# Kernel tuning notes

Measured on AMD Instinct MI355X. Metric: run time of the kernel, lower is better.

The kernel has to match this reference:

```python
import jax, jax.numpy as jnp
import numpy as np

B, L, H, R = 8, 128, 768, 24


def setup_inputs() -> dict:
    key = jax.random.key(0)
    ks = jax.random.split(key, 12)
    s = 0.02  # init scale
    f32 = jnp.float32
    inp = {
        "embed_tokens": jax.random.normal(ks[0], (B, L, H), f32),
        "attention_mask": jnp.ones((B, L), f32),
        "target_rel": jax.random.randint(ks[1], (B,), 0, R),
        # relation-judgement head
        "W_hr": jax.random.normal(ks[2], (H, H // 2), f32) * s,
        "b_hr": jnp.zeros((H // 2,), f32),
        "W_rj": jax.random.normal(ks[3], (H // 2, R), f32) * s,
        "b_rj": jnp.zeros((R,), f32),
        # relation embedding
        "rel_emb": jax.random.normal(ks[4], (R, H), f32) * s,
        # correspondence matrix head (input is concat -> 2H)
        "W_corr": jax.random.normal(ks[5], (2 * H, H), f32) * s,
        "b_corr": jnp.zeros((H,), f32),
        "W_gc": jax.random.normal(ks[6], (H, 1), f32) * s,
        "b_gc": jnp.zeros((1,), f32),
        # subject tagging head (fusion_type='concat' -> 2H in, H hidden)
        "W_sh": jax.random.normal(ks[7], (2 * H, H), f32) * s,
        "b_sh": jnp.zeros((H,), f32),
        "W_st": jax.random.normal(ks[8], (H, 3), f32) * s,
        "b_st": jnp.zeros((3,), f32),
        # object tagging head
        "W_oh": jax.random.normal(ks[9], (2 * H, H), f32) * s,
        "b_oh": jnp.zeros((H,), f32),
        "W_ot": jax.random.normal(ks[10], (H, 3), f32) * s,
        "b_ot": jnp.zeros((3,), f32),
    }
    return inp


def reference(embed_tokens, attention_mask, target_rel,
              W_hr, b_hr, W_rj, b_rj, rel_emb,
              W_corr, b_corr, W_gc, b_gc,
              W_sh, b_sh, W_st, b_st,
              W_oh, b_oh, W_ot, b_ot):
    # ---- stage 1: masked mean-pool + relation judgement (dropout = identity at inference)
    masked = embed_tokens * attention_mask[:, :, None]            # [B,L,H]
    pool = jnp.sum(masked, axis=1) / jnp.sum(attention_mask, axis=1)[:, None]  # [B,H]
    rel_hidden = jax.nn.relu(pool @ W_hr + b_hr)                  # [B,H/2]
    stage1 = rel_hidden @ W_rj + b_rj                             # [B,R]

    # ---- correspondence matrix: concat[b,i,j] = [embed[b,j], embed[b,i]]
    # Decompose concat-linear: concat @ W_corr = embed_j @ W1 + embed_i @ W2
    W1, W2 = W_corr[:H_dim(embed_tokens)], W_corr[H_dim(embed_tokens):]
    A = embed_tokens @ W1                                         # [B,L,H] (j-index part)
    C = embed_tokens @ W2                                         # [B,L,H] (i-index part)
    corres_hidden = jax.nn.relu(A[:, None, :, :] + C[:, :, None, :] + b_corr)  # [B,L,L,H]
    pred_corres = corres_hidden @ W_gc + b_gc                     # [B,L,L,1]

    # ---- relation-fused tagging (mode == 'train')
    re = rel_emb[target_rel]                                      # [B,H]
    Bsz, Lsz, Hsz = embed_tokens.shape
    fusion = jnp.concatenate(
        [jnp.broadcast_to(re[:, None, :], (Bsz, Lsz, Hsz)), embed_tokens], axis=-1)  # [B,L,2H]
    subj = jax.nn.relu(fusion @ W_sh + b_sh) @ W_st + b_st        # [B,L,3]
    obj = jax.nn.relu(fusion @ W_oh + b_oh) @ W_ot + b_ot         # [B,L,3]

    return stage1, subj, obj, pred_corres


def H_dim(x):
    return x.shape[-1]
```

## Files before the change

kernel.cpp:

```cpp
#include <hip/hip_runtime.h>
#include <hip/hip_bf16.h>

#define BD   8
#define LD   128
#define HD   768
#define RD   24
#define H2D  384
#define NF   1536
#define WSZ  589824

typedef __attribute__((ext_vector_type(8))) short bf16x8;
typedef __attribute__((ext_vector_type(4))) float f32x4;

__device__ __forceinline__ short f2bf(float f) {
    __hip_bfloat16 h = __float2bfloat16(f);
    return *reinterpret_cast<short*>(&h);
}

__global__ __launch_bounds__(256) void prep_kernel(
        const float* __restrict__ embed, const float* __restrict__ mask,
        const float* __restrict__ rel_emb, const int* __restrict__ trel,
        const float* __restrict__ W_corr,
        const float* __restrict__ W_sh, const float* __restrict__ b_sh,
        const float* __restrict__ W_oh, const float* __restrict__ b_oh,
        const float* __restrict__ b_st, const float* __restrict__ b_ot,
        float* __restrict__ pool, float* __restrict__ biasrel,
        unsigned short* __restrict__ embedB, unsigned short* __restrict__ WT,
        float* __restrict__ out_subj, float* __restrict__ out_obj) {
    const int q = blockIdx.x, tid = threadIdx.x;

    if (q < 96) {
        const int b = q / 12, c = q % 12;
        __shared__ float mrow[LD];
        __shared__ float msum;
        __shared__ float part[4][64];
        if (tid < LD) mrow[tid] = mask[b * LD + tid];
        __syncthreads();
        if (tid == 0) {
            float s = 0.f;
            for (int l = 0; l < LD; ++l) s += mrow[l];
            msum = s;
        }
        __syncthreads();
        const int lc = tid >> 6, hh = tid & 63;
        const int h = c * 64 + hh;
        float acc = 0.f;
        const float* base = embed + ((size_t)b * LD + lc * 32) * HD + h;
#pragma unroll 8
        for (int i = 0; i < 32; ++i) acc += base[(size_t)i * HD] * mrow[lc * 32 + i];
        part[lc][hh] = acc;
        __syncthreads();
        if (lc == 0)
            pool[b * HD + h] = (part[0][hh] + part[1][hh] + part[2][hh] + part[3][hh]) / msum;
    } else if (q < 192) {
        const int qq = q - 96;
        const int b = qq / 12, cc = qq % 12;
        __shared__ float re[HD];
        __shared__ float part2[2][128];
        const int rel = trel[b];
        for (int k = tid; k < HD; k += 256) re[k] = rel_emb[(size_t)rel * HD + k];
        if (qq == 0 && tid < 3 * LD) {
            const int l = tid / 3, t = tid - 3 * l;
            out_subj[(l) * 3 + t] = b_st[t];
            out_obj [(l) * 3 + t] = b_ot[t];
        }
        if (cc == 0 && b > 0 && tid < 3 * LD) {
            const int l = tid / 3, t = tid - 3 * l;
            out_subj[(b * LD + l) * 3 + t] = b_st[t];
            out_obj [(b * LD + l) * 3 + t] = b_ot[t];
        }
        __syncthreads();
        const int kc = tid >> 7, nn = tid & 127;
        const int n = cc * 128 + nn;
        const float* Wp; float bb; int col;
        if (n < HD) { Wp = W_sh; bb = b_sh[n];      col = n; }
        else        { Wp = W_oh; bb = b_oh[n - HD]; col = n - HD; }
        float acc = 0.f;
#pragma unroll 8
        for (int i = 0; i < 384; ++i) {
            const int k = kc * 384 + i;
            acc += re[k] * Wp[(size_t)k * HD + col];
        }
        part2[kc][nn] = acc;
        __syncthreads();
        if (kc == 0) biasrel[b * NF + n] = part2[0][nn] + part2[1][nn] + bb;
    } else if (q < 288) {
        const int base = (q - 192) * 8192;
#pragma unroll
        for (int it = 0; it < 4; ++it) {
            const int off = base + it * 2048 + tid * 8;
            float4 v0 = *(const float4*)&embed[off];
            float4 v1 = *(const float4*)&embed[off + 4];
            bf16x8 p;
            p[0] = f2bf(v0.x); p[1] = f2bf(v0.y); p[2] = f2bf(v0.z); p[3] = f2bf(v0.w);
            p[4] = f2bf(v1.x); p[5] = f2bf(v1.y); p[6] = f2bf(v1.z); p[7] = f2bf(v1.w);
            *(bf16x8*)&embedB[off] = p;
        }
    } else {
        const int qq = q - 288;
        const int w = qq / 144, t = qq % 144;
        const int kt = t / 12, nt = t % 12;
        const float* src = (w == 0) ? W_corr
                         : (w == 1) ? W_corr + WSZ
                         : (w == 2) ? W_sh + WSZ
                                    : W_oh + WSZ;
        unsigned short* dst = WT + (size_t)w * WSZ;
        __shared__ float tile[64 * 65];
        const int r = tid >> 2, c4 = (tid & 3) * 16;
#pragma unroll
        for (int i = 0; i < 4; ++i) {
            float4 v = *(const float4*)&src[(size_t)(kt * 64 + r) * HD + nt * 64 + c4 + i * 4];
            tile[r * 65 + c4 + i * 4 + 0] = v.x;
            tile[r * 65 + c4 + i * 4 + 1] = v.y;
            tile[r * 65 + c4 + i * 4 + 2] = v.z;
            tile[r * 65 + c4 + i * 4 + 3] = v.w;
        }
        __syncthreads();
        bf16x8 p0, p1;
#pragma unroll
        for (int j = 0; j < 8; ++j) {
            p0[j] = f2bf(tile[(c4 + j) * 65 + r]);
            p1[j] = f2bf(tile[(c4 + 8 + j) * 65 + r]);
        }
        unsigned short* o = dst + (size_t)(nt * 64 + r) * HD + kt * 64 + c4;
        *(bf16x8*)(o)     = p0;
        *(bf16x8*)(o + 8) = p1;
    }
}

__global__ __launch_bounds__(256) void biggemm(
        const unsigned short* __restrict__ embedB,
        const unsigned short* __restrict__ WT,
        const float* __restrict__ biasrel,
        const float* __restrict__ W_st, const float* __restrict__ W_ot,
        const float* __restrict__ pool,
        const float* __restrict__ W_hr, const float* __restrict__ b_hr,
        float* __restrict__ AC, float* __restrict__ out_subj,
        float* __restrict__ out_obj, float* __restrict__ rh) {
    const int tid = threadIdx.x;

    if (blockIdx.x >= 24) {
        const int b = blockIdx.y >> 1;
        const int c = (blockIdx.x - 24) * 2 + (blockIdx.y & 1);
        __shared__ float prow[HD];
        __shared__ float rpart[4][64];
        for (int k = tid; k < HD; k += 256) prow[k] = pool[b * HD + k];
        __syncthreads();
        const int kc = tid >> 6, nn = tid & 63;
        const int n = c * 64 + nn;
        float acc = 0.f;
#pragma unroll 8
        for (int i = 0; i < 192; ++i) {
            const int k = kc * 192 + i;
            acc += prow[k] * W_hr[(size_t)k * H2D + n];
        }
        rpart[kc][nn] = acc;
        __syncthreads();
        if (kc == 0)
            rh[b * H2D + n] = fmaxf(rpart[0][nn] + rpart[1][nn] + rpart[2][nn] + rpart[3][nn] + b_hr[n], 0.f);
        return;
    }

    __shared__ __align__(16) short As [64][40];
    __shared__ __align__(16) short Bs0[64][40];
    __shared__ __align__(16) short Bs1[64][40];
    __shared__ float partial[64][3];

    const int bn0 = blockIdx.x * 64;
    const int bm0 = blockIdx.y * 64;

    const unsigned short* W0 = (bn0 < HD) ? WT : WT + WSZ;
    const unsigned short* W1 = (bn0 < HD) ? WT + 2 * (size_t)WSZ : WT + 3 * (size_t)WSZ;
    const int col0 = (bn0 < HD) ? bn0 : bn0 - HD;

    if (tid < 192) partial[tid / 3][tid % 3] = 0.f;

    const int row = tid >> 2;
    const int kc8 = (tid & 3) * 8;

    const int lane = tid & 63;
    const int wv = tid >> 6;
    const int wm = (wv >> 1) * 32;
    const int wn = (wv & 1) * 32;
    const int fr = lane & 15;
    const int kq = (lane >> 4) * 8;
    const int mq = (lane >> 4) * 4;

    f32x4 c00 = {0.f,0.f,0.f,0.f}, c01 = c00, c10 = c00, c11 = c00;
    f32x4 h00 = c00, h01 = c00, h10 = c00, h11 = c00;

    for (int kt = 0; kt < 24; ++kt) {
        const int k0 = kt << 5;
        bf16x8 av = *(const bf16x8*)&embedB[(size_t)(bm0 + row) * HD + k0 + kc8];
        bf16x8 b0v = *(const bf16x8*)&W0[(size_t)(col0 + row) * HD + k0 + kc8];
        bf16x8 b1v = *(const bf16x8*)&W1[(size_t)(col0 + row) * HD + k0 + kc8];

        __syncthreads();
        *(bf16x8*)&As [row][kc8] = av;
        *(bf16x8*)&Bs0[row][kc8] = b0v;
        *(bf16x8*)&Bs1[row][kc8] = b1v;
        __syncthreads();

        bf16x8 a0 = *(bf16x8*)&As[wm + fr][kq];
        bf16x8 a1 = *(bf16x8*)&As[wm + 16 + fr][kq];
        bf16x8 b0 = *(bf16x8*)&Bs0[wn + fr][kq];
        bf16x8 b1 = *(bf16x8*)&Bs0[wn + 16 + fr][kq];
        bf16x8 d0 = *(bf16x8*)&Bs1[wn + fr][kq];
        bf16x8 d1 = *(bf16x8*)&Bs1[wn + 16 + fr][kq];
        c00 = __builtin_amdgcn_mfma_f32_16x16x32_bf16(a0, b0, c00, 0, 0, 0);
        c01 = __builtin_amdgcn_mfma_f32_16x16x32_bf16(a0, b1, c01, 0, 0, 0);
        c10 = __builtin_amdgcn_mfma_f32_16x16x32_bf16(a1, b0, c10, 0, 0, 0);
        c11 = __builtin_amdgcn_mfma_f32_16x16x32_bf16(a1, b1, c11, 0, 0, 0);
        h00 = __builtin_amdgcn_mfma_f32_16x16x32_bf16(a0, d0, h00, 0, 0, 0);
        h01 = __builtin_amdgcn_mfma_f32_16x16x32_bf16(a0, d1, h01, 0, 0, 0);
        h10 = __builtin_amdgcn_mfma_f32_16x16x32_bf16(a1, d0, h10, 0, 0, 0);
        h11 = __builtin_amdgcn_mfma_f32_16x16x32_bf16(a1, d1, h11, 0, 0, 0);
    }

#pragma unroll
    for (int i = 0; i < 2; ++i) {
#pragma unroll
        for (int j = 0; j < 2; ++j) {
            f32x4 a = (i == 0) ? (j == 0 ? c00 : c01) : (j == 0 ? c10 : c11);
            const int ncol = bn0 + wn + j * 16 + fr;
#pragma unroll
            for (int r = 0; r < 4; ++r) {
                const int mrow = bm0 + wm + i * 16 + mq + r;
                AC[(size_t)mrow * NF + ncol] = a[r];
            }
        }
    }

    {
        const float* brl = biasrel + (size_t)(bm0 / LD) * NF;
        const float* Wt = (bn0 < HD) ? W_st : W_ot;
        float* op = (bn0 < HD) ? out_subj : out_obj;
        float pt[8][3] = {};
#pragma unroll
        for (int j = 0; j < 2; ++j) {
            const int ncol = bn0 + wn + j * 16 + fr;
            const int ncl = (bn0 < HD) ? ncol : ncol - HD;
            const float wt0 = Wt[ncl * 3 + 0];
            const float wt1 = Wt[ncl * 3 + 1];
            const float wt2 = Wt[ncl * 3 + 2];
            const float bias = brl[ncol];
#pragma unroll
            for (int i = 0; i < 2; ++i) {
                f32x4 a = (i == 0) ? (j == 0 ? h00 : h01) : (j == 0 ? h10 : h11);
#pragma unroll
                for (int r = 0; r < 4; ++r) {
                    const float v = fmaxf(a[r] + bias, 0.f);
                    pt[i * 4 + r][0] += v * wt0;
                    pt[i * 4 + r][1] += v * wt1;
                    pt[i * 4 + r][2] += v * wt2;
                }
            }
        }
#pragma unroll
        for (int mask = 1; mask < 16; mask <<= 1) {
#pragma unroll
            for (int x = 0; x < 8; ++x)
#pragma unroll
                for (int t = 0; t < 3; ++t)
                    pt[x][t] += __shfl_xor(pt[x][t], mask, 64);
        }
        if (fr == 0) {
#pragma unroll
            for (int i = 0; i < 2; ++i)
#pragma unroll
                for (int r = 0; r < 4; ++r)
#pragma unroll
                    for (int t = 0; t < 3; ++t)
                        atomicAdd(&partial[wm + i * 16 + mq + r][t], pt[i * 4 + r][t]);
        }
        __syncthreads();
        if (tid < 192) {
            const int m = tid / 3, t = tid % 3;
            atomicAdd(&op[(size_t)(bm0 + m) * 3 + t], partial[m][t]);
        }
    }
}

__global__ __launch_bounds__(512) void corres_kernel(
        const float* __restrict__ AC,
        const float* __restrict__ b_corr, const float* __restrict__ W_gc,
        const float* __restrict__ b_gc,
        const float* __restrict__ rh,
        const float* __restrict__ W_rj, const float* __restrict__ b_rj,
        float* __restrict__ out, float* __restrict__ out_stage1) {
    const int b = blockIdx.y;
    const int tid = threadIdx.x;

    if (blockIdx.x == 32) {
        __shared__ float rl[H2D];
        __shared__ float spart[8][RD];
        if (tid < H2D) rl[tid] = rh[b * H2D + tid];
        __syncthreads();
        if (tid < 8 * RD) {
            const int n = tid % RD, kc = tid / RD;
            float acc = 0.f;
#pragma unroll 8
            for (int i = 0; i < 48; ++i) {
                const int k = kc * 48 + i;
                acc += rl[k] * W_rj[k * RD + n];
            }
            spart[kc][n] = acc;
        }
        __syncthreads();
        if (tid < RD) {
            float s = b_rj[tid];
#pragma unroll
            for (int q = 0; q < 8; ++q) s += spart[q][tid];
            out_stage1[b * RD + tid] = s;
        }
        return;
    }

    const int i0 = blockIdx.x * 4;
    const int lane = tid & 63;
    const int wave = tid >> 6;

    f32x4 wg[3], cb[4][3];
#pragma unroll
    for (int s = 0; s < 3; ++s) {
        const int h = s * 256 + lane * 4;
        f32x4 w = *(const f32x4*)&W_gc[h];
        f32x4 bc = *(const f32x4*)&b_corr[h];
        wg[s] = w;
#pragma unroll
        for (int i = 0; i < 4; ++i) {
            f32x4 cv = *(const f32x4*)&AC[((size_t)(b * LD + i0 + i)) * NF + HD + h];
            cb[i][s] = cv + bc;
        }
    }
    const float bg = b_gc[0];

    for (int j = wave; j < LD; j += 8) {
        const float* arow = AC + ((size_t)(b * LD + j)) * NF;
        f32x4 a[3];
#pragma unroll
        for (int s = 0; s < 3; ++s) a[s] = *(const f32x4*)&arow[s * 256 + lane * 4];
        float sum[4] = {0.f, 0.f, 0.f, 0.f};
#pragma unroll
        for (int s = 0; s < 3; ++s) {
#pragma unroll
            for (int i = 0; i < 4; ++i) {
                f32x4 v = a[s] + cb[i][s];
#pragma unroll
                for (int t = 0; t < 4; ++t)
                    sum[i] += fmaxf(v[t], 0.f) * wg[s][t];
            }
        }
#pragma unroll
        for (int off = 32; off > 0; off >>= 1) {
#pragma unroll
            for (int i = 0; i < 4; ++i) sum[i] += __shfl_down(sum[i], off, 64);
        }
        if (lane == 0) {
#pragma unroll
            for (int i = 0; i < 4; ++i)
                out[((size_t)(b * LD + i0 + i)) * LD + j] = sum[i] + bg;
        }
    }
}

extern "C" void kernel_launch(void* const* d_in, const int* in_sizes, int n_in,
                              void* d_out, int out_size, void* d_ws, size_t ws_size,
                              hipStream_t stream) {
    const float* embed   = (const float*)d_in[0];
    const float* mask    = (const float*)d_in[1];
    const int*   trel    = (const int*)d_in[2];
    const float* W_hr    = (const float*)d_in[3];
    const float* b_hr    = (const float*)d_in[4];
    const float* W_rj    = (const float*)d_in[5];
    const float* b_rj    = (const float*)d_in[6];
    const float* rel_emb = (const float*)d_in[7];
    const float* W_corr  = (const float*)d_in[8];
    const float* b_corr  = (const float*)d_in[9];
    const float* W_gc    = (const float*)d_in[10];
    const float* b_gc    = (const float*)d_in[11];
    const float* W_sh    = (const float*)d_in[12];
    const float* b_sh    = (const float*)d_in[13];
    const float* W_st    = (const float*)d_in[14];
    const float* b_st    = (const float*)d_in[15];
    const float* W_oh    = (const float*)d_in[16];
    const float* b_oh    = (const float*)d_in[17];
    const float* W_ot    = (const float*)d_in[18];
    const float* b_ot    = (const float*)d_in[19];
    float* out = (float*)d_out;

    float* ws      = (float*)d_ws;
    float* AC      = ws;
    float* biasrel = ws + 1572864;
    float* rh      = ws + 1572864 + 12288;
    float* pool    = ws + 1572864 + 12288 + 3072;
    unsigned short* embedB = (unsigned short*)(ws + 1594368);
    unsigned short* WT     = (unsigned short*)(ws + 1594368 + 393216);

    float* out_stage1 = out;
    float* out_subj   = out + 192;
    float* out_obj    = out + 3264;
    float* out_corr   = out + 6336;

    prep_kernel<<<864, 256, 0, stream>>>(embed, mask, rel_emb, trel, W_corr,
                                         W_sh, b_sh, W_oh, b_oh, b_st, b_ot,
                                         pool, biasrel, embedB, WT,
                                         out_subj, out_obj);

    biggemm<<<dim3(27, 16), 256, 0, stream>>>(embedB, WT, biasrel, W_st, W_ot,
                                              pool, W_hr, b_hr,
                                              AC, out_subj, out_obj, rh);

    corres_kernel<<<dim3(33, BD), 512, 0, stream>>>(AC, b_corr, W_gc, b_gc,
                                                    rh, W_rj, b_rj, out_corr, out_stage1);
}
```

Measured before the change: 161.1 us.

## Fuse three kernels into one cooperative persistent kernel with grid syncs

Replaces the prep, GEMM and correspondence launches with a single cooperative kernel of 256 blocks that loops over the work units and uses grid-wide syncs between phases. If the cooperative launch fails, it falls back to three separate kernels. The correspondence stage also drops from 512 to 256 threads and prefetches the next AC row in registers. This removes launch gaps and tail effects, at the cost of fewer resident blocks per phase and the overhead of grid sync.

```diff
diff --git a/kernel.cpp b/kernel.cpp
--- a/kernel.cpp
+++ b/kernel.cpp
@@ -1,5 +1,8 @@
 #include <hip/hip_runtime.h>
 #include <hip/hip_bf16.h>
+#include <hip/hip_cooperative_groups.h>
+
+namespace cg = cooperative_groups;
 
 #define BD   8
 #define LD   128
@@ -17,110 +20,112 @@
     return *reinterpret_cast<short*>(&h);
 }
 
-__global__ __launch_bounds__(256) void prep_kernel(
-        const float* __restrict__ embed, const float* __restrict__ mask,
-        const float* __restrict__ rel_emb, const int* __restrict__ trel,
-        const float* __restrict__ W_corr,
-        const float* __restrict__ W_sh, const float* __restrict__ b_sh,
-        const float* __restrict__ W_oh, const float* __restrict__ b_oh,
-        const float* __restrict__ b_st, const float* __restrict__ b_ot,
-        float* __restrict__ pool, float* __restrict__ biasrel,
-        unsigned short* __restrict__ embedB, unsigned short* __restrict__ WT,
-        float* __restrict__ out_subj, float* __restrict__ out_obj) {
-    const int q = blockIdx.x, tid = threadIdx.x;
-
+struct KParams {
+    const float *embed, *mask;
+    const int *trel;
+    const float *W_hr, *b_hr, *W_rj, *b_rj, *rel_emb, *W_corr;
+    const float *b_corr, *W_gc, *b_gc;
+    const float *W_sh, *b_sh, *W_st, *b_st, *W_oh, *b_oh, *W_ot, *b_ot;
+    float *AC, *biasrel, *rh, *pool;
+    unsigned short *embedB, *WT;
+    float *out_stage1, *out_subj, *out_obj, *out_corr;
+};
+
+union SMem {
+    struct { float mrow[LD]; float msum; float part[4][64]; } pl;
+    struct { float re[HD]; float part2[2][128]; } br;
+    float tile[64 * 65];
+    struct __align__(16) { short As[64][40]; short Bs0[64][40]; short Bs1[64][40];
+                           float partial[64][3]; } gm;
+    struct { float prow[HD]; float rpart[4][64]; } rl;
+    struct { float rlb[H2D]; float spart[8][RD]; } st;
+};
+
+__device__ void prep_unit(const KParams& p, SMem& sm, int q, int tid) {
     if (q < 96) {
         const int b = q / 12, c = q % 12;
-        __shared__ float mrow[LD];
-        __shared__ float msum;
-        __shared__ float part[4][64];
-        if (tid < LD) mrow[tid] = mask[b * LD + tid];
+        if (tid < LD) sm.pl.mrow[tid] = p.mask[b * LD + tid];
         __syncthreads();
         if (tid == 0) {
             float s = 0.f;
-            for (int l = 0; l < LD; ++l) s += mrow[l];
-            msum = s;
+            for (int l = 0; l < LD; ++l) s += sm.pl.mrow[l];
+            sm.pl.msum = s;
         }
         __syncthreads();
         const int lc = tid >> 6, hh = tid & 63;
         const int h = c * 64 + hh;
         float acc = 0.f;
-        const float* base = embed + ((size_t)b * LD + lc * 32) * HD + h;
+        const float* base = p.embed + ((size_t)b * LD + lc * 32) * HD + h;
 #pragma unroll 8
-        for (int i = 0; i < 32; ++i) acc += base[(size_t)i * HD] * mrow[lc * 32 + i];
-        part[lc][hh] = acc;
+        for (int i = 0; i < 32; ++i) acc += base[(size_t)i * HD] * sm.pl.mrow[lc * 32 + i];
+        sm.pl.part[lc][hh] = acc;
         __syncthreads();
         if (lc == 0)
-            pool[b * HD + h] = (part[0][hh] + part[1][hh] + part[2][hh] + part[3][hh]) / msum;
+            p.pool[b * HD + h] = (sm.pl.part[0][hh] + sm.pl.part[1][hh] +
+                                  sm.pl.part[2][hh] + sm.pl.part[3][hh]) / sm.pl.msum;
     } else if (q < 192) {
         const int qq = q - 96;
         const int b = qq / 12, cc = qq % 12;
-        __shared__ float re[HD];
-        __shared__ float part2[2][128];
-        const int rel = trel[b];
-        for (int k = tid; k < HD; k += 256) re[k] = rel_emb[(size_t)rel * HD + k];
-        if (qq == 0 && tid < 3 * LD) {
-            const int l = tid / 3, t = tid - 3 * l;
-            out_subj[(l) * 3 + t] = b_st[t];
-            out_obj [(l) * 3 + t] = b_ot[t];
-        }
-        if (cc == 0 && b > 0 && tid < 3 * LD) {
-            const int l = tid / 3, t = tid - 3 * l;
-            out_subj[(b * LD + l) * 3 + t] = b_st[t];
-            out_obj [(b * LD + l) * 3 + t] = b_ot[t];
+        const int rel = p.trel[b];
+        for (int k = tid; k < HD; k += 256) sm.br.re[k] = p.rel_emb[(size_t)rel * HD + k];
+        if (cc == 0) {
+            for (int u = tid; u < 3 * LD; u += 256) {
+                const int l = u / 3, t = u - 3 * l;
+                p.out_subj[(b * LD + l) * 3 + t] = p.b_st[t];
+                p.out_obj [(b * LD + l) * 3 + t] = p.b_ot[t];
+            }
         }
         __syncthreads();
         const int kc = tid >> 7, nn = tid & 127;
         const int n = cc * 128 + nn;
         const float* Wp; float bb; int col;
-        if (n < HD) { Wp = W_sh; bb = b_sh[n];      col = n; }
-        else        { Wp = W_oh; bb = b_oh[n - HD]; col = n - HD; }
+        if (n < HD) { Wp = p.W_sh; bb = p.b_sh[n];      col = n; }
+        else        { Wp = p.W_oh; bb = p.b_oh[n - HD]; col = n - HD; }
         float acc = 0.f;
 #pragma unroll 8
         for (int i = 0; i < 384; ++i) {
             const int k = kc * 384 + i;
-            acc += re[k] * Wp[(size_t)k * HD + col];
-        }
-        part2[kc][nn] = acc;
-        __syncthreads();
-        if (kc == 0) biasrel[b * NF + n] = part2[0][nn] + part2[1][nn] + bb;
+            acc += sm.br.re[k] * Wp[(size_t)k * HD + col];
+        }
+        sm.br.part2[kc][nn] = acc;
+        __syncthreads();
+        if (kc == 0) p.biasrel[b * NF + n] = sm.br.part2[0][nn] + sm.br.part2[1][nn] + bb;
     } else if (q < 288) {
         const int base = (q - 192) * 8192;
 #pragma unroll
         for (int it = 0; it < 4; ++it) {
             const int off = base + it * 2048 + tid * 8;
-            float4 v0 = *(const float4*)&embed[off];
-            float4 v1 = *(const float4*)&embed[off + 4];
-            bf16x8 p;
-            p[0] = f2bf(v0.x); p[1] = f2bf(v0.y); p[2] = f2bf(v0.z); p[3] = f2bf(v0.w);
-            p[4] = f2bf(v1.x); p[5] = f2bf(v1.y); p[6] = f2bf(v1.z); p[7] = f2bf(v1.w);
-            *(bf16x8*)&embedB[off] = p;
+            float4 v0 = *(const float4*)&p.embed[off];
+            float4 v1 = *(const float4*)&p.embed[off + 4];
+            bf16x8 pk;
+            pk[0] = f2bf(v0.x); pk[1] = f2bf(v0.y); pk[2] = f2bf(v0.z); pk[3] = f2bf(v0.w);
+            pk[4] = f2bf(v1.x); pk[5] = f2bf(v1.y); pk[6] = f2bf(v1.z); pk[7] = f2bf(v1.w);
+            *(bf16x8*)&p.embedB[off] = pk;
         }
     } else {
         const int qq = q - 288;
         const int w = qq / 144, t = qq % 144;
         const int kt = t / 12, nt = t % 12;
-        const float* src = (w == 0) ? W_corr
-                         : (w == 1) ? W_corr + WSZ
-                         : (w == 2) ? W_sh + WSZ
-                                    : W_oh + WSZ;
-        unsigned short* dst = WT + (size_t)w * WSZ;
-        __shared__ float tile[64 * 65];
+        const float* src = (w == 0) ? p.W_corr
+                         : (w == 1) ? p.W_corr + WSZ
+                         : (w == 2) ? p.W_sh + WSZ
+                                    : p.W_oh + WSZ;
+        unsigned short* dst = p.WT + (size_t)w * WSZ;
         const int r = tid >> 2, c4 = (tid & 3) * 16;
 #pragma unroll
         for (int i = 0; i < 4; ++i) {
             float4 v = *(const float4*)&src[(size_t)(kt * 64 + r) * HD + nt * 64 + c4 + i * 4];
-            tile[r * 65 + c4 + i * 4 + 0] = v.x;
-            tile[r * 65 + c4 + i * 4 + 1] = v.y;
-            tile[r * 65 + c4 + i * 4 + 2] = v.z;
-            tile[r * 65 + c4 + i * 4 + 3] = v.w;
+            sm.tile[r * 65 + c4 + i * 4 + 0] = v.x;
+            sm.tile[r * 65 + c4 + i * 4 + 1] = v.y;
+            sm.tile[r * 65 + c4 + i * 4 + 2] = v.z;
+            sm.tile[r * 65 + c4 + i * 4 + 3] = v.w;
         }
         __syncthreads();
         bf16x8 p0, p1;
 #pragma unroll
         for (int j = 0; j < 8; ++j) {
-            p0[j] = f2bf(tile[(c4 + j) * 65 + r]);
-            p1[j] = f2bf(tile[(c4 + 8 + j) * 65 + r]);
+            p0[j] = f2bf(sm.tile[(c4 + j) * 65 + r]);
+            p1[j] = f2bf(sm.tile[(c4 + 8 + j) * 65 + r]);
         }
         unsigned short* o = dst + (size_t)(nt * 64 + r) * HD + kt * 64 + c4;
         *(bf16x8*)(o)     = p0;
@@ -128,56 +133,18 @@
     }
 }
 
-__global__ __launch_bounds__(256) void biggemm(
-        const unsigned short* __restrict__ embedB,
-        const unsigned short* __restrict__ WT,
-        const float* __restrict__ biasrel,
-        const float* __restrict__ W_st, const float* __restrict__ W_ot,
-        const float* __restrict__ pool,
-        const float* __restrict__ W_hr, const float* __restrict__ b_hr,
-        float* __restrict__ AC, float* __restrict__ out_subj,
-        float* __restrict__ out_obj, float* __restrict__ rh) {
-    const int tid = threadIdx.x;
-
-    if (blockIdx.x >= 24) {
-        const int b = blockIdx.y >> 1;
-        const int c = (blockIdx.x - 24) * 2 + (blockIdx.y & 1);
-        __shared__ float prow[HD];
-        __shared__ float rpart[4][64];
-        for (int k = tid; k < HD; k += 256) prow[k] = pool[b * HD + k];
-        __syncthreads();
-        const int kc = tid >> 6, nn = tid & 63;
-        const int n = c * 64 + nn;
-        float acc = 0.f;
-#pragma unroll 8
-        for (int i = 0; i < 192; ++i) {
-            const int k = kc * 192 + i;
-            acc += prow[k] * W_hr[(size_t)k * H2D + n];
-        }
-        rpart[kc][nn] = acc;
-        __syncthreads();
-        if (kc == 0)
-            rh[b * H2D + n] = fmaxf(rpart[0][nn] + rpart[1][nn] + rpart[2][nn] + rpart[3][nn] + b_hr[n], 0.f);
-        return;
-    }
-
-    __shared__ __align__(16) short As [64][40];
-    __shared__ __align__(16) short Bs0[64][40];
-    __shared__ __align__(16) short Bs1[64][40];
-    __shared__ float partial[64][3];
-
-    const int bn0 = blockIdx.x * 64;
-    const int bm0 = blockIdx.y * 64;
-
-    const unsigned short* W0 = (bn0 < HD) ? WT : WT + WSZ;
-    const unsigned short* W1 = (bn0 < HD) ? WT + 2 * (size_t)WSZ : WT + 3 * (size_t)WSZ;
+__device__ void gemm_unit(const KParams& p, SMem& sm, int u, int tid) {
+    const int bn0 = (u % 24) * 64;
+    const int bm0 = (u / 24) * 64;
+
+    const unsigned short* W0 = (bn0 < HD) ? p.WT : p.WT + WSZ;
+    const unsigned short* W1 = (bn0 < HD) ? p.WT + 2 * (size_t)WSZ : p.WT + 3 * (size_t)WSZ;
     const int col0 = (bn0 < HD) ? bn0 : bn0 - HD;
 
-    if (tid < 192) partial[tid / 3][tid % 3] = 0.f;
+    if (tid < 192) sm.gm.partial[tid / 3][tid % 3] = 0.f;
 
     const int row = tid >> 2;
     const int kc8 = (tid & 3) * 8;
-
     const int lane = tid & 63;
     const int wv = tid >> 6;
     const int wm = (wv >> 1) * 32;
@@ -191,22 +158,22 @@
 
     for (int kt = 0; kt < 24; ++kt) {
         const int k0 = kt << 5;
-        bf16x8 av = *(const bf16x8*)&embedB[(size_t)(bm0 + row) * HD + k0 + kc8];
+        bf16x8 av  = *(const bf16x8*)&p.embedB[(size_t)(bm0 + row) * HD + k0 + kc8];
         bf16x8 b0v = *(const bf16x8*)&W0[(size_t)(col0 + row) * HD + k0 + kc8];
         bf16x8 b1v = *(const bf16x8*)&W1[(size_t)(col0 + row) * HD + k0 + kc8];
 
         __syncthreads();
-        *(bf16x8*)&As [row][kc8] = av;
-        *(bf16x8*)&Bs0[row][kc8] = b0v;
-        *(bf16x8*)&Bs1[row][kc8] = b1v;
-        __syncthreads();
-
-        bf16x8 a0 = *(bf16x8*)&As[wm + fr][kq];
-        bf16x8 a1 = *(bf16x8*)&As[wm + 16 + fr][kq];
-        bf16x8 b0 = *(bf16x8*)&Bs0[wn + fr][kq];
-        bf16x8 b1 = *(bf16x8*)&Bs0[wn + 16 + fr][kq];
-        bf16x8 d0 = *(bf16x8*)&Bs1[wn + fr][kq];
-        bf16x8 d1 = *(bf16x8*)&Bs1[wn + 16 + fr][kq];
+        *(bf16x8*)&sm.gm.As [row][kc8] = av;
+        *(bf16x8*)&sm.gm.Bs0[row][kc8] = b0v;
+        *(bf16x8*)&sm.gm.Bs1[row][kc8] = b1v;
+        __syncthreads();
+
+        bf16x8 a0 = *(bf16x8*)&sm.gm.As[wm + fr][kq];
+        bf16x8 a1 = *(bf16x8*)&sm.gm.As[wm + 16 + fr][kq];
+        bf16x8 b0 = *(bf16x8*)&sm.gm.Bs0[wn + fr][kq];
+        bf16x8 b1 = *(bf16x8*)&sm.gm.Bs0[wn + 16 + fr][kq];
+        bf16x8 d0 = *(bf16x8*)&sm.gm.Bs1[wn + fr][kq];
+        bf16x8 d1 = *(bf16x8*)&sm.gm.Bs1[wn + 16 + fr][kq];
         c00 = __builtin_amdgcn_mfma_f32_16x16x32_bf16(a0, b0, c00, 0, 0, 0);
         c01 = __builtin_amdgcn_mfma_f32_16x16x32_bf16(a0, b1, c01, 0, 0, 0);
         c10 = __builtin_amdgcn_mfma_f32_16x16x32_bf16(a1, b0, c10, 0, 0, 0);
@@ -226,15 +193,15 @@
 #pragma unroll
             for (int r = 0; r < 4; ++r) {
                 const int mrow = bm0 + wm + i * 16 + mq + r;
-                AC[(size_t)mrow * NF + ncol] = a[r];
+                p.AC[(size_t)mrow * NF + ncol] = a[r];
             }
         }
     }
 
     {
-        const float* brl = biasrel + (size_t)(bm0 / LD) * NF;
-        const float* Wt = (bn0 < HD) ? W_st : W_ot;
-        float* op = (bn0 < HD) ? out_subj : out_obj;
+        const float* brl = p.biasrel + (size_t)(bm0 / LD) * NF;
+        const float* Wt = (bn0 < HD) ? p.W_st : p.W_ot;
+        float* op = (bn0 < HD) ? p.out_subj : p.out_obj;
         float pt[8][3] = {};
 #pragma unroll
         for (int j = 0; j < 2; ++j) {
@@ -271,52 +238,38 @@
                 for (int r = 0; r < 4; ++r)
 #pragma unroll
                     for (int t = 0; t < 3; ++t)
-                        atomicAdd(&partial[wm + i * 16 + mq + r][t], pt[i * 4 + r][t]);
+                        atomicAdd(&sm.gm.partial[wm + i * 16 + mq + r][t], pt[i * 4 + r][t]);
         }
         __syncthreads();
         if (tid < 192) {
             const int m = tid / 3, t = tid % 3;
-            atomicAdd(&op[(size_t)(bm0 + m) * 3 + t], partial[m][t]);
-        }
-    }
-}
-
-__global__ __launch_bounds__(512) void corres_kernel(
-        const float* __restrict__ AC,
-        const float* __restrict__ b_corr, const float* __restrict__ W_gc,
-        const float* __restrict__ b_gc,
-        const float* __restrict__ rh,
-        const float* __restrict__ W_rj, const float* __restrict__ b_rj,
-        float* __restrict__ out, float* __restrict__ out_stage1) {
-    const int b = blockIdx.y;
-    const int tid = threadIdx.x;
-
-    if (blockIdx.x == 32) {
-        __shared__ float rl[H2D];
-        __shared__ float spart[8][RD];
-        if (tid < H2D) rl[tid] = rh[b * H2D + tid];
-        __syncthreads();
-        if (tid < 8 * RD) {
-            const int n = tid % RD, kc = tid / RD;
-            float acc = 0.f;
+            atomicAdd(&op[(size_t)(bm0 + m) * 3 + t], sm.gm.partial[m][t]);
+        }
+    }
+}
+
+__device__ void relh_unit(const KParams& p, SMem& sm, int u, int tid) {
+    const int b = u / 6, c = u % 6;
+    for (int k = tid; k < HD; k += 256) sm.rl.prow[k] = p.pool[b * HD + k];
+    __syncthreads();
+    const int kc = tid >> 6, nn = tid & 63;
+    const int n = c * 64 + nn;
+    float acc = 0.f;
 #pragma unroll 8
-            for (int i = 0; i < 48; ++i) {
-                const int k = kc * 48 + i;
-                acc += rl[k] * W_rj[k * RD + n];
-            }
-            spart[kc][n] = acc;
-        }
-        __syncthreads();
-        if (tid < RD) {
-            float s = b_rj[tid];
-#pragma unroll
-            for (int q = 0; q < 8; ++q) s += spart[q][tid];
-            out_stage1[b * RD + tid] = s;
-        }
-        return;
-    }
-
-    const int i0 = blockIdx.x * 4;
+    for (int i = 0; i < 192; ++i) {
+        const int k = kc * 192 + i;
+        acc += sm.rl.prow[k] * p.W_hr[(size_t)k * H2D + n];
+    }
+    sm.rl.rpart[kc][nn] = acc;
+    __syncthreads();
+    if (kc == 0)
+        p.rh[b * H2D + n] = fmaxf(sm.rl.rpart[0][nn] + sm.rl.rpart[1][nn] +
+                                  sm.rl.rpart[2][nn] + sm.rl.rpart[3][nn] + p.b_hr[n], 0.f);
+}
+
+__device__ void corres_unit(const KParams& p, int u, int tid) {
+    const int b = u >> 5;
+    const int i0 = (u & 31) * 4;
     const int lane = tid & 63;
     const int wave = tid >> 6;
 
@@ -324,22 +277,30 @@
 #pragma unroll
     for (int s = 0; s < 3; ++s) {
         const int h = s * 256 + lane * 4;
-        f32x4 w = *(const f32x4*)&W_gc[h];
-        f32x4 bc = *(const f32x4*)&b_corr[h];
+        f32x4 w  = *(const f32x4*)&p.W_gc[h];
+        f32x4 bc = *(const f32x4*)&p.b_corr[h];
         wg[s] = w;
 #pragma unroll
         for (int i = 0; i < 4; ++i) {
-            f32x4 cv = *(const f32x4*)&AC[((size_t)(b * LD + i0 + i)) * NF + HD + h];
+            f32x4 cv = *(const f32x4*)&p.AC[((size_t)(b * LD + i0 + i)) * NF + HD + h];
             cb[i][s] = cv + bc;
         }
     }
-    const float bg = b_gc[0];
-
-    for (int j = wave; j < LD; j += 8) {
-        const float* arow = AC + ((size_t)(b * LD + j)) * NF;
-        f32x4 a[3];
-#pragma unroll
-        for (int s = 0; s < 3; ++s) a[s] = *(const f32x4*)&arow[s * 256 + lane * 4];
+    const float bg = p.b_gc[0];
+
+    f32x4 a[3];
+    {
+        const float* ar = p.AC + ((size_t)(b * LD + wave)) * NF;
+#pragma unroll
+        for (int s = 0; s < 3; ++s) a[s] = *(const f32x4*)&ar[s * 256 + lane * 4];
+    }
+    for (int j = wave; j < LD; j += 4) {
+        f32x4 an[3];
+        if (j + 4 < LD) {
+            const float* ar = p.AC + ((size_t)(b * LD + j + 4)) * NF;
+#pragma unroll
+            for (int s = 0; s < 3; ++s) an[s] = *(const f32x4*)&ar[s * 256 + lane * 4];
+        }
         float sum[4] = {0.f, 0.f, 0.f, 0.f};
 #pragma unroll
         for (int s = 0; s < 3; ++s) {
@@ -359,58 +320,129 @@
         if (lane == 0) {
 #pragma unroll
             for (int i = 0; i < 4; ++i)
-                out[((size_t)(b * LD + i0 + i)) * LD + j] = sum[i] + bg;
-        }
-    }
+                p.out_corr[((size_t)(b * LD + i0 + i)) * LD + j] = sum[i] + bg;
+        }
+#pragma unroll
+        for (int s = 0; s < 3; ++s) a[s] = an[s];
+    }
+}
+
+__device__ void stage1_unit(const KParams& p, SMem& sm, int b, int tid) {
+    for (int k = tid; k < H2D; k += 256) sm.st.rlb[k] = p.rh[b * H2D + k];
+    __syncthreads();
+    if (tid < 8 * RD) {
+        const int n = tid % RD, kc = tid / RD;
+        float acc = 0.f;
+#pragma unroll 8
+        for (int i = 0; i < 48; ++i) {
+            const int k = kc * 48 + i;
+            acc += sm.st.rlb[k] * p.W_rj[k * RD + n];
+        }
+        sm.st.spart[kc][n] = acc;
+    }
+    __syncthreads();
+    if (tid < RD) {
+        float s = p.b_rj[tid];
+#pragma unroll
+        for (int q = 0; q < 8; ++q) s += sm.st.spart[q][tid];
+        p.out_stage1[b * RD + tid] = s;
+    }
+}
+
+__global__ __launch_bounds__(256) void mega(KParams p) {
+    __shared__ SMem sm;
+    const int blk = blockIdx.x;
+    const int tid = threadIdx.x;
+    cg::grid_group grid = cg::this_grid();
+
+    prep_unit(p, sm, blk, tid);
+    for (int q = blk + 256; q < 864; q += 256) {
+        __syncthreads();
+        prep_unit(p, sm, q, tid);
+    }
+    __threadfence();
+    grid.sync();
+
+    if (blk < 384) gemm_unit(p, sm, blk, tid);
+    else           relh_unit(p, sm, blk - 384, tid);
+    if (blk < 176) {
+        __syncthreads();
+        const int u2 = blk + 256;
+        if (u2 < 384) gemm_unit(p, sm, u2, tid);
+        else          relh_unit(p, sm, u2 - 384, tid);
+    }
+    __threadfence();
+    grid.sync();
+
+    if (blk >= 248) stage1_unit(p, sm, blk - 248, tid);
+    __syncthreads();
+    corres_unit(p, blk, tid);
+}
+
+__global__ __launch_bounds__(256) void prep_k(KParams p) {
+    __shared__ SMem sm;
+    prep_unit(p, sm, blockIdx.x, threadIdx.x);
+}
+__global__ __launch_bounds__(256) void phaseB_k(KParams p) {
+    __shared__ SMem sm;
+    const int u = blockIdx.x;
+    if (u < 384) gemm_unit(p, sm, u, threadIdx.x);
+    else         relh_unit(p, sm, u - 384, threadIdx.x);
+}
+__global__ __launch_bounds__(256) void phaseC_k(KParams p) {
+    __shared__ SMem sm;
+    const int u = blockIdx.x;
+    if (u < 256) corres_unit(p, u, threadIdx.x);
+    else         stage1_unit(p, sm, u - 256, threadIdx.x);
 }
 
 extern "C" void kernel_launch(void* const* d_in, const int* in_sizes, int n_in,
                               void* d_out, int out_size, void* d_ws, size_t ws_size,
                               hipStream_t stream) {
-    const float* embed   = (const float*)d_in[0];
-    const float* mask    = (const float*)d_in[1];
-    const int*   trel    = (const int*)d_in[2];
-    const float* W_hr    = (const float*)d_in[3];
-    const float* b_hr    = (const float*)d_in[4];
-    const float* W_rj    = (const float*)d_in[5];
-    const float* b_rj    = (const float*)d_in[6];
-    const float* rel_emb = (const float*)d_in[7];
-    const float* W_corr  = (const float*)d_in[8];
-    const float* b_corr  = (const float*)d_in[9];
-    const float* W_gc    = (const float*)d_in[10];
-    const float* b_gc    = (const float*)d_in[11];
-    const float* W_sh    = (const float*)d_in[12];
-    const float* b_sh    = (const float*)d_in[13];
-    const float* W_st    = (const float*)d_in[14];
-    const float* b_st    = (const float*)d_in[15];
-    const float* W_oh    = (const float*)d_in[16];
-    const float* b_oh    = (const float*)d_in[17];
-    const float* W_ot    = (const float*)d_in[18];
-    const float* b_ot    = (const float*)d_in[19];
     float* out = (float*)d_out;
-
-    float* ws      = (float*)d_ws;
-    float* AC      = ws;
-    float* biasrel = ws + 1572864;
-    float* rh      = ws + 1572864 + 12288;
-    float* pool    = ws + 1572864 + 12288 + 3072;
-    unsigned short* embedB = (unsigned short*)(ws + 1594368);
-    unsigned short* WT     = (unsigned short*)(ws + 1594368 + 393216);
-
-    float* out_stage1 = out;
-    float* out_subj   = out + 192;
-    float* out_obj    = out + 3264;
-    float* out_corr   = out + 6336;
-
-    prep_kernel<<<864, 256, 0, stream>>>(embed, mask, rel_emb, trel, W_corr,
-                                         W_sh, b_sh, W_oh, b_oh, b_st, b_ot,
-                                         pool, biasrel, embedB, WT,
-                                         out_subj, out_obj);
-
-    biggemm<<<dim3(27, 16), 256, 0, stream>>>(embedB, WT, biasrel, W_st, W_ot,
-                                              pool, W_hr, b_hr,
-                                              AC, out_subj, out_obj, rh);
-
-    corres_kernel<<<dim3(33, BD), 512, 0, stream>>>(AC, b_corr, W_gc, b_gc,
-                                                    rh, W_rj, b_rj, out_corr, out_stage1);
-}
+    float* ws  = (float*)d_ws;
+
+    KParams p;
+    p.embed   = (const float*)d_in[0];
+    p.mask    = (const float*)d_in[1];
+    p.trel    = (const int*)d_in[2];
+    p.W_hr    = (const float*)d_in[3];
+    p.b_hr    = (const float*)d_in[4];
+    p.W_rj    = (const float*)d_in[5];
+    p.b_rj    = (const float*)d_in[6];
+    p.rel_emb = (const float*)d_in[7];
+    p.W_corr  = (const float*)d_in[8];
+    p.b_corr  = (const float*)d_in[9];
+    p.W_gc    = (const float*)d_in[10];
+    p.b_gc    = (const float*)d_in[11];
+    p.W_sh    = (const float*)d_in[12];
+    p.b_sh    = (const float*)d_in[13];
+    p.W_st    = (const float*)d_in[14];
+    p.b_st    = (const float*)d_in[15];
+    p.W_oh    = (const float*)d_in[16];
+    p.b_oh    = (const float*)d_in[17];
+    p.W_ot    = (const float*)d_in[18];
+    p.b_ot    = (const float*)d_in[19];
+
+    p.AC      = ws;
+    p.biasrel = ws + 1572864;
+    p.rh      = ws + 1572864 + 12288;
+    p.pool    = ws + 1572864 + 12288 + 3072;
+    p.embedB  = (unsigned short*)(ws + 1594368);
+    p.WT      = (unsigned short*)(ws + 1594368 + 393216);
+
+    p.out_stage1 = out;
+    p.out_subj   = out + 192;
+    p.out_obj    = out + 3264;
+    p.out_corr   = out + 6336;
+
+    void* args[] = { (void*)&p };
+    hipError_t e = hipLaunchCooperativeKernel((const void*)mega, dim3(256), dim3(256),
+                                              args, 0u, stream);
+    if (e != hipSuccess) {
+        (void)hipGetLastError();
+        prep_k<<<864, 256, 0, stream>>>(p);
+        phaseB_k<<<432, 256, 0, stream>>>(p);
+        phaseC_k<<<264, 256, 0, stream>>>(p);
+    }
+}
```

After: 317.2 us. +96.9%, slower.
